# Optimization experiments

Hardware: AMD Instinct MI355X
Metric: run time of the kernel (lower is better)

## Reference

```python
import jax, jax.numpy as jnp
import numpy as np

E = 1_000_000
C = 32
OUT = 64


def setup_inputs() -> dict:
    key = jax.random.key(0)
    k_x, k_nb, k_w, k_b = jax.random.split(key, 4)
    x = jax.random.normal(k_x, (E, C), dtype=jnp.float32)
    neighbors = jax.random.randint(k_nb, (E, 4), 0, E, dtype=jnp.int64)
    # Linear(5*C, OUT): weight [OUT, 5C], bias [OUT] (torch layout)
    bound = 1.0 / np.sqrt(5 * C)
    W = jax.random.uniform(k_w, (OUT, 5 * C), minval=-bound, maxval=bound, dtype=jnp.float32)
    b = jax.random.uniform(k_b, (OUT,), minval=-bound, maxval=bound, dtype=jnp.float32)
    return {"x": x, "neighbors": neighbors, "W": W, "b": b}


def reference(x, neighbors, W, b):
    # pad with a zero row so index -1 (clamped to 0 then masked) yields zeros
    padded = jnp.concatenate([x, jnp.zeros((1, x.shape[1]), dtype=x.dtype)], axis=0)
    safe = jnp.clip(neighbors, 0, None)
    nb = padded[safe]                                  # [E, 4, C]
    nb = jnp.where((neighbors < 0)[..., None], 0.0, nb)
    a0, a1, b0, b1 = nb[:, 0], nb[:, 1], nb[:, 2], nb[:, 3]
    desc_a = jnp.concatenate([a0 + a1, jnp.abs(a0 - a1)], axis=1)   # [E, 2C]
    desc_b = jnp.concatenate([b0 + b1, jnp.abs(b0 - b1)], axis=1)   # [E, 2C]
    combined = jnp.concatenate([x, desc_a + desc_b, jnp.abs(desc_a - desc_b)], axis=1)  # [E, 5C]
    return combined @ W.T + b
```

## Files before the change

### kernel.cpp

```cpp
#include <hip/hip_runtime.h>


typedef __bf16 bf16_t;
typedef __bf16 bf16x8 __attribute__((ext_vector_type(8)));
typedef float  f32x4  __attribute__((ext_vector_type(4)));

#define EC      1000000
#define CCH     32
#define OUTD    64
#define KD      160
#define MT      64
#define LSTR    168
#define NTILES  (EC / MT)

__global__ __launch_bounds__(256)
void meshconv_kernel(const float* __restrict__ x,
                     const int*   __restrict__ nbr,
                     const float* __restrict__ W,
                     const float* __restrict__ bias,
                     float*       __restrict__ out)
{
    __shared__ bf16_t w_lds[OUTD * LSTR];
    __shared__ bf16_t c_lds[MT * LSTR];

    const int tid  = threadIdx.x;
    const int wave = tid >> 6;
    const int lane = tid & 63;
    const int col  = lane & 15;
    const int quad = lane >> 4;

    for (int i = tid; i < (OUTD * KD) / 4; i += 256) {
        const int row = i / 40;
        const int c4  = (i - row * 40) * 4;
        f32x4 wv = ((const f32x4*)W)[i];
        bf16_t* d = &w_lds[row * LSTR + c4];
        d[0] = (bf16_t)wv[0]; d[1] = (bf16_t)wv[1];
        d[2] = (bf16_t)wv[2]; d[3] = (bf16_t)wv[3];
    }

    float bv[4];
#pragma unroll
    for (int tn = 0; tn < 4; ++tn) bv[tn] = bias[tn * 16 + col];

    const int e_loc = tid >> 2;
    const int part  = tid & 3;

    for (int tile = blockIdx.x; tile < NTILES; tile += (int)gridDim.x) {
        const int e = tile * MT + e_loc;

        const int4 nb = ((const int4*)nbr)[e];
        const float m0 = nb.x < 0 ? 0.f : 1.f;
        const float m1 = nb.y < 0 ? 0.f : 1.f;
        const float m2 = nb.z < 0 ? 0.f : 1.f;
        const float m3 = nb.w < 0 ? 0.f : 1.f;
        const int i0 = nb.x < 0 ? 0 : nb.x;
        const int i1 = nb.y < 0 ? 0 : nb.y;
        const int i2 = nb.z < 0 ? 0 : nb.z;
        const int i3 = nb.w < 0 ? 0 : nb.w;

        const f32x4* px  = (const f32x4*)(x + (size_t)e  * CCH) + part * 2;
        const f32x4* pa0 = (const f32x4*)(x + (size_t)i0 * CCH) + part * 2;
        const f32x4* pa1 = (const f32x4*)(x + (size_t)i1 * CCH) + part * 2;
        const f32x4* pb0 = (const f32x4*)(x + (size_t)i2 * CCH) + part * 2;
        const f32x4* pb1 = (const f32x4*)(x + (size_t)i3 * CCH) + part * 2;

        f32x4 xv[2], a0[2], a1[2], b0[2], b1[2];
#pragma unroll
        for (int h = 0; h < 2; ++h) {
            xv[h] = px[h];
            a0[h] = pa0[h] * m0;
            a1[h] = pa1[h] * m1;
            b0[h] = pb0[h] * m2;
            b1[h] = pb1[h] * m3;
        }

        bf16x8 vx, v1, v2, v3, v4;
#pragma unroll
        for (int h = 0; h < 2; ++h) {
#pragma unroll
            for (int j = 0; j < 4; ++j) {
                const int jj = h * 4 + j;
                const float sa = a0[h][j] + a1[h][j];
                const float da = fabsf(a0[h][j] - a1[h][j]);
                const float sb = b0[h][j] + b1[h][j];
                const float db = fabsf(b0[h][j] - b1[h][j]);
                vx[jj] = (bf16_t)xv[h][j];
                v1[jj] = (bf16_t)(sa + sb);
                v2[jj] = (bf16_t)(da + db);
                v3[jj] = (bf16_t)fabsf(sa - sb);
                v4[jj] = (bf16_t)fabsf(da - db);
            }
        }

        bf16_t* rowp = &c_lds[e_loc * LSTR + part * 8];
        *(bf16x8*)(rowp +   0) = vx;
        *(bf16x8*)(rowp +  32) = v1;
        *(bf16x8*)(rowp +  64) = v2;
        *(bf16x8*)(rowp +  96) = v3;
        *(bf16x8*)(rowp + 128) = v4;

        __syncthreads();

        f32x4 acc[4] = {{0.f,0.f,0.f,0.f},{0.f,0.f,0.f,0.f},
                        {0.f,0.f,0.f,0.f},{0.f,0.f,0.f,0.f}};
#pragma unroll
        for (int ks = 0; ks < 5; ++ks) {
            const bf16x8 af = *(const bf16x8*)&c_lds[(wave * 16 + col) * LSTR + ks * 32 + quad * 8];
#pragma unroll
            for (int tn = 0; tn < 4; ++tn) {
                const bf16x8 bfr = *(const bf16x8*)&w_lds[(tn * 16 + col) * LSTR + ks * 32 + quad * 8];
                acc[tn] = __builtin_amdgcn_mfma_f32_16x16x32_bf16(af, bfr, acc[tn], 0, 0, 0);
            }
        }

#pragma unroll
        for (int tn = 0; tn < 4; ++tn) {
            float* op = out + (size_t)(tile * MT + wave * 16 + quad * 4) * OUTD + tn * 16 + col;
#pragma unroll
            for (int r = 0; r < 4; ++r)
                op[(size_t)r * OUTD] = acc[tn][r] + bv[tn];
        }

        __syncthreads();
    }
}

extern "C" void kernel_launch(void* const* d_in, const int* in_sizes, int n_in,
                              void* d_out, int out_size, void* d_ws, size_t ws_size,
                              hipStream_t stream) {
    const float* x    = (const float*)d_in[0];
    const int*   nbr  = (const int*)d_in[1];
    const float* W    = (const float*)d_in[2];
    const float* bias = (const float*)d_in[3];
    float* out = (float*)d_out;
    meshconv_kernel<<<dim3(768), dim3(256), 0, stream>>>(x, nbr, W, bias, out);
}
```

Before: 419.6 us.

## Build MFMA A-fragments in registers and pre-swizzle weights into fragment order

Measured after the change: 436.6 us. +4.0%, slower.

```diff
diff --git a/kernel.cpp b/kernel.cpp
--- a/kernel.cpp
+++ b/kernel.cpp
@@ -10,8 +10,8 @@
 #define OUTD    64
 #define KD      160
 #define MT      64
-#define LSTR    168
 #define NTILES  (EC / MT)
+#define NFRAG   1280
 
 __global__ __launch_bounds__(256)
 void meshconv_kernel(const float* __restrict__ x,
@@ -20,8 +20,7 @@
                      const float* __restrict__ bias,
                      float*       __restrict__ out)
 {
-    __shared__ bf16_t w_lds[OUTD * LSTR];
-    __shared__ bf16_t c_lds[MT * LSTR];
+    __shared__ bf16_t w_lds[NFRAG * 8];
 
     const int tid  = threadIdx.x;
     const int wave = tid >> 6;
@@ -29,24 +28,28 @@
     const int col  = lane & 15;
     const int quad = lane >> 4;
 
-    for (int i = tid; i < (OUTD * KD) / 4; i += 256) {
-        const int row = i / 40;
-        const int c4  = (i - row * 40) * 4;
-        f32x4 wv = ((const f32x4*)W)[i];
-        bf16_t* d = &w_lds[row * LSTR + c4];
-        d[0] = (bf16_t)wv[0]; d[1] = (bf16_t)wv[1];
-        d[2] = (bf16_t)wv[2]; d[3] = (bf16_t)wv[3];
+    for (int i = tid; i < NFRAG; i += 256) {
+        const int fc  = i & 15;
+        const int fq  = (i >> 4) & 3;
+        const int ftn = (i >> 6) & 3;
+        const int fks = i >> 8;
+        const float* src = W + (ftn * 16 + fc) * KD + fks * 32 + fq * 8;
+        f32x4 w0 = *(const f32x4*)src;
+        f32x4 w1 = *(const f32x4*)(src + 4);
+        bf16x8 wf;
+        wf[0]=(bf16_t)w0[0]; wf[1]=(bf16_t)w0[1]; wf[2]=(bf16_t)w0[2]; wf[3]=(bf16_t)w0[3];
+        wf[4]=(bf16_t)w1[0]; wf[5]=(bf16_t)w1[1]; wf[6]=(bf16_t)w1[2]; wf[7]=(bf16_t)w1[3];
+        *(bf16x8*)&w_lds[i * 8] = wf;
     }
 
     float bv[4];
 #pragma unroll
     for (int tn = 0; tn < 4; ++tn) bv[tn] = bias[tn * 16 + col];
 
-    const int e_loc = tid >> 2;
-    const int part  = tid & 3;
+    __syncthreads();
 
     for (int tile = blockIdx.x; tile < NTILES; tile += (int)gridDim.x) {
-        const int e = tile * MT + e_loc;
+        const int e = tile * MT + wave * 16 + col;
 
         const int4 nb = ((const int4*)nbr)[e];
         const float m0 = nb.x < 0 ? 0.f : 1.f;
@@ -58,11 +61,12 @@
         const int i2 = nb.z < 0 ? 0 : nb.z;
         const int i3 = nb.w < 0 ? 0 : nb.w;
 
-        const f32x4* px  = (const f32x4*)(x + (size_t)e  * CCH) + part * 2;
-        const f32x4* pa0 = (const f32x4*)(x + (size_t)i0 * CCH) + part * 2;
-        const f32x4* pa1 = (const f32x4*)(x + (size_t)i1 * CCH) + part * 2;
-        const f32x4* pb0 = (const f32x4*)(x + (size_t)i2 * CCH) + part * 2;
-        const f32x4* pb1 = (const f32x4*)(x + (size_t)i3 * CCH) + part * 2;
+        const int co = quad * 8;
+        const f32x4* px  = (const f32x4*)(x + (size_t)e  * CCH + co);
+        const f32x4* pa0 = (const f32x4*)(x + (size_t)i0 * CCH + co);
+        const f32x4* pa1 = (const f32x4*)(x + (size_t)i1 * CCH + co);
+        const f32x4* pb0 = (const f32x4*)(x + (size_t)i2 * CCH + co);
+        const f32x4* pb1 = (const f32x4*)(x + (size_t)i3 * CCH + co);
 
         f32x4 xv[2], a0[2], a1[2], b0[2], b1[2];
 #pragma unroll
@@ -74,7 +78,7 @@
             b1[h] = pb1[h] * m3;
         }
 
-        bf16x8 vx, v1, v2, v3, v4;
+        bf16x8 af[5];
 #pragma unroll
         for (int h = 0; h < 2; ++h) {
 #pragma unroll
@@ -84,32 +88,22 @@
                 const float da = fabsf(a0[h][j] - a1[h][j]);
                 const float sb = b0[h][j] + b1[h][j];
                 const float db = fabsf(b0[h][j] - b1[h][j]);
-                vx[jj] = (bf16_t)xv[h][j];
-                v1[jj] = (bf16_t)(sa + sb);
-                v2[jj] = (bf16_t)(da + db);
-                v3[jj] = (bf16_t)fabsf(sa - sb);
-                v4[jj] = (bf16_t)fabsf(da - db);
+                af[0][jj] = (bf16_t)xv[h][j];
+                af[1][jj] = (bf16_t)(sa + sb);
+                af[2][jj] = (bf16_t)(da + db);
+                af[3][jj] = (bf16_t)fabsf(sa - sb);
+                af[4][jj] = (bf16_t)fabsf(da - db);
             }
         }
-
-        bf16_t* rowp = &c_lds[e_loc * LSTR + part * 8];
-        *(bf16x8*)(rowp +   0) = vx;
-        *(bf16x8*)(rowp +  32) = v1;
-        *(bf16x8*)(rowp +  64) = v2;
-        *(bf16x8*)(rowp +  96) = v3;
-        *(bf16x8*)(rowp + 128) = v4;
-
-        __syncthreads();
 
         f32x4 acc[4] = {{0.f,0.f,0.f,0.f},{0.f,0.f,0.f,0.f},
                         {0.f,0.f,0.f,0.f},{0.f,0.f,0.f,0.f}};
 #pragma unroll
         for (int ks = 0; ks < 5; ++ks) {
-            const bf16x8 af = *(const bf16x8*)&c_lds[(wave * 16 + col) * LSTR + ks * 32 + quad * 8];
 #pragma unroll
             for (int tn = 0; tn < 4; ++tn) {
-                const bf16x8 bfr = *(const bf16x8*)&w_lds[(tn * 16 + col) * LSTR + ks * 32 + quad * 8];
-                acc[tn] = __builtin_amdgcn_mfma_f32_16x16x32_bf16(af, bfr, acc[tn], 0, 0, 0);
+                const bf16x8 bfr = *(const bf16x8*)&w_lds[(((ks*4+tn)*4+quad)*16 + col) * 8];
+                acc[tn] = __builtin_amdgcn_mfma_f32_16x16x32_bf16(af[ks], bfr, acc[tn], 0, 0, 0);
             }
         }
 
@@ -118,10 +112,8 @@
             float* op = out + (size_t)(tile * MT + wave * 16 + quad * 4) * OUTD + tn * 16 + col;
 #pragma unroll
             for (int r = 0; r < 4; ++r)
-                op[(size_t)r * OUTD] = acc[tn][r] + bv[tn];
+                __builtin_nontemporal_store(acc[tn][r] + bv[tn], op + (size_t)r * OUTD);
         }
-
-        __syncthreads();
     }
 }
 
@@ -133,5 +125,5 @@
     const float* W    = (const float*)d_in[2];
     const float* bias = (const float*)d_in[3];
     float* out = (float*)d_out;
-    meshconv_kernel<<<dim3(768), dim3(256), 0, stream>>>(x, nbr, W, bias, out);
+    meshconv_kernel<<<dim3(3072), dim3(256), 0, stream>>>(x, nbr, W, bias, out);
 }
```
